# Kernel optimization log

Hardware: AMD Instinct MI355X
Metric: run time of the kernel (lower is better)

Reference implementation:

```python
import jax, jax.numpy as jnp
import numpy as np

D = 1024
NUM_ITERS = 3
EPS = 1e-6
SCALE = D ** -0.5


def rmsnorm(x, w, eps=EPS):
    return x * jax.lax.rsqrt(jnp.mean(x * x, axis=-1, keepdims=True) + eps) * w


def setup_inputs() -> dict:
    key = jax.random.key(0)
    ks = jax.random.split(key, 8)
    B, K, M, d = 8, 64, 4096, D
    w_std = d ** -0.5
    return {
        "slots": jax.random.normal(ks[0], (B, K, d), jnp.float32),
        "P": jax.random.normal(ks[1], (B, M, d), jnp.float32),
        "Wq": jax.random.normal(ks[2], (d, d), jnp.float32) * w_std,
        "Wk": jax.random.normal(ks[3], (d, d), jnp.float32) * w_std,
        "Wv": jax.random.normal(ks[4], (d, d), jnp.float32) * w_std,
        "gru_wih": jax.random.normal(ks[5], (3 * d, d), jnp.float32) * w_std,
        "gru_whh": jax.random.normal(ks[6], (3 * d, d), jnp.float32) * w_std,
        "gru_bih": jnp.zeros((3 * d,), jnp.float32),
        "gru_bhh": jnp.zeros((3 * d,), jnp.float32),
        "slot_norm_w": jnp.ones((d,), jnp.float32),
        "input_norm_w": jnp.ones((d,), jnp.float32),
    }


def gru_cell(x, h, wih, whh, bih, bhh):
    # PyTorch nn.GRUCell semantics; x, h: (..., d)
    gx = x @ wih.T + bih            # (..., 3d)
    gh = h @ whh.T + bhh
    xr, xz, xn = jnp.split(gx, 3, axis=-1)
    hr, hz, hn = jnp.split(gh, 3, axis=-1)
    r = jax.nn.sigmoid(xr + hr)
    z = jax.nn.sigmoid(xz + hz)
    n = jnp.tanh(xn + r * hn)
    return (1.0 - z) * n + z * h


def reference(slots, P, Wq, Wk, Wv, gru_wih, gru_whh, gru_bih, gru_bhh,
              slot_norm_w, input_norm_w):
    Pn = rmsnorm(P, input_norm_w)
    k_proj = Pn @ Wk.T              # (B, M, d)  (qk_layernorm=False -> identity)
    v_proj = Pn @ Wv.T              # (B, M, d)
    for _ in range(NUM_ITERS):
        sn = rmsnorm(slots, slot_norm_w)
        q_proj = sn @ Wq.T          # (B, K, d)
        scores = jnp.einsum("bkd,bmd->bkm", q_proj, k_proj) * SCALE
        attn = jax.nn.softmax(scores, axis=-2)              # compete over slots K
        attn = attn / (jnp.sum(attn, axis=-1, keepdims=True) + EPS)
        updates = jnp.einsum("bkm,bmd->bkd", attn, v_proj)
        slots = gru_cell(updates, slots, gru_wih, gru_whh, gru_bih, gru_bhh)
    return slots
```

## Files before the change

### kernel.cpp

```cpp
#include <hip/hip_runtime.h>
#include <stdint.h>

typedef _Float16 f16;
typedef __attribute__((ext_vector_type(4))) _Float16 f16x4;
typedef __attribute__((ext_vector_type(8))) _Float16 f16x8;
typedef __attribute__((ext_vector_type(4))) float f32x4;

#define EPSF 1e-6f

using as1_cvoid = const __attribute__((address_space(1))) void;
using as3_void  = __attribute__((address_space(3))) void;

__device__ __forceinline__ float blockReduceSum256(float v) {
#pragma unroll
  for (int o = 32; o > 0; o >>= 1) v += __shfl_down(v, o);
  __shared__ float red[4];
  int lane = threadIdx.x & 63, wid = threadIdx.x >> 6;
  if (lane == 0) red[wid] = v;
  __syncthreads();
  return red[0] + red[1] + red[2] + red[3];
}

__global__ __launch_bounds__(256) void cvt_f32_f16(const float* __restrict__ src,
                                                   f16* __restrict__ dst, int n) {
  int i = (blockIdx.x * 256 + threadIdx.x) * 4;
  if (i >= n) return;
  float4 v = *(const float4*)(src + i);
  f16x4 o = {(f16)v.x, (f16)v.y, (f16)v.z, (f16)v.w};
  *(f16x4*)(dst + i) = o;
}

__global__ __launch_bounds__(256) void rmsnorm_rows(const float* __restrict__ X,
                                                    const float* __restrict__ w,
                                                    f16* __restrict__ Y) {
  const size_t row = blockIdx.x;
  const int t = threadIdx.x;
  float4 v = ((const float4*)(X + row * 1024))[t];
  float tot = blockReduceSum256(v.x * v.x + v.y * v.y + v.z * v.z + v.w * v.w);
  float s = rsqrtf(tot * (1.0f / 1024.0f) + EPSF);
  float4 wv = ((const float4*)w)[t];
  f16x4 o = {(f16)(v.x * s * wv.x), (f16)(v.y * s * wv.y),
             (f16)(v.z * s * wv.z), (f16)(v.w * s * wv.w)};
  *(f16x4*)(Y + row * 1024 + t * 4) = o;
}

__global__ __launch_bounds__(256) void slots_prep(const float* __restrict__ S,
                                                  const float* __restrict__ w,
                                                  f16* __restrict__ sn,
                                                  f16* __restrict__ sraw,
                                                  float* __restrict__ rowsum) {
  const size_t row = blockIdx.x;
  const int t = threadIdx.x;
  if (t == 0) rowsum[row] = 0.f;
  float4 v = ((const float4*)(S + row * 1024))[t];
  float tot = blockReduceSum256(v.x * v.x + v.y * v.y + v.z * v.z + v.w * v.w);
  float s = rsqrtf(tot * (1.0f / 1024.0f) + EPSF);
  float4 wv = ((const float4*)w)[t];
  f16x4 a = {(f16)(v.x * s * wv.x), (f16)(v.y * s * wv.y),
             (f16)(v.z * s * wv.z), (f16)(v.w * s * wv.w)};
  f16x4 b = {(f16)v.x, (f16)v.y, (f16)v.z, (f16)v.w};
  *(f16x4*)(sn + row * 1024 + t * 4) = a;
  *(f16x4*)(sraw + row * 1024 + t * 4) = b;
}

__global__ __launch_bounds__(512) void gemm_kv(
    const f16* __restrict__ Pn, const f16* __restrict__ Wk, const f16* __restrict__ Wv,
    f16* __restrict__ kproj, f16* __restrict__ vT) {
  __shared__ f16 Al[128 * 32];
  __shared__ f16 Bkv[2][128 * 32];
  const int tid = threadIdx.x;
  const int wave = tid >> 6, lane = tid & 63;
  const int id = blockIdx.x;
  const int xcd = id & 7, slot = id >> 3;
  const int nx = slot & 7;
  const int my = xcd * 32 + (slot >> 3);
  const int m0 = my * 128, n0 = nx * 128;
  const int wsel = wave >> 2;
  const int w4 = wave & 3;
  const int wm = w4 >> 1, wn = w4 & 1;
  const int cr = lane & 15, kseg = lane >> 4;

  f32x4 acc[4][4];
  f32x4 vzero = {0.f, 0.f, 0.f, 0.f};
#pragma unroll
  for (int i = 0; i < 4; ++i)
#pragma unroll
    for (int j = 0; j < 4; ++j) acc[i][j] = vzero;

  const int off = wave * 1024 + lane * 16;
  const int sr = off >> 6, scb = off & 63;
  for (int kt = 0; kt < 32; ++kt) {
    const int k0 = kt << 5;
    {
      const char* src = (const char*)(Pn + (size_t)(m0 + sr) * 1024 + k0) + scb;
      __builtin_amdgcn_global_load_lds((as1_cvoid*)src,
                                       (as3_void*)((char*)Al + wave * 1024), 16, 0, 0);
    }
    {
      const char* src = (const char*)(Wk + (size_t)(n0 + sr) * 1024 + k0) + scb;
      __builtin_amdgcn_global_load_lds((as1_cvoid*)src,
                                       (as3_void*)((char*)&Bkv[0][0] + wave * 1024), 16, 0, 0);
    }
    {
      const char* src = (const char*)(Wv + (size_t)(n0 + sr) * 1024 + k0) + scb;
      __builtin_amdgcn_global_load_lds((as1_cvoid*)src,
                                       (as3_void*)((char*)&Bkv[1][0] + wave * 1024), 16, 0, 0);
    }
    __syncthreads();
    f16x8 af[4], bf[4];
#pragma unroll
    for (int i = 0; i < 4; ++i)
      af[i] = *(const f16x8*)&Al[(wm * 64 + i * 16 + cr) * 32 + kseg * 8];
#pragma unroll
    for (int j = 0; j < 4; ++j)
      bf[j] = *(const f16x8*)&Bkv[wsel][(wn * 64 + j * 16 + cr) * 32 + kseg * 8];
#pragma unroll
    for (int i = 0; i < 4; ++i)
#pragma unroll
      for (int j = 0; j < 4; ++j)
        acc[i][j] = __builtin_amdgcn_mfma_f32_16x16x32_f16(af[i], bf[j], acc[i][j], 0, 0, 0);
    __syncthreads();
  }

  const int cq4 = kseg * 4;
  if (wsel == 0) {
#pragma unroll
    for (int i = 0; i < 4; ++i) {
      const int rb = m0 + wm * 64 + i * 16 + cq4;
#pragma unroll
      for (int j = 0; j < 4; ++j) {
        const int gn = n0 + wn * 64 + j * 16 + cr;
#pragma unroll
        for (int r = 0; r < 4; ++r)
          kproj[(size_t)(rb + r) * 1024 + gn] = (f16)acc[i][j][r];
      }
    }
  } else {
#pragma unroll
    for (int i = 0; i < 4; ++i) {
      const int gm = m0 + wm * 64 + i * 16 + cq4;
      const int b = gm >> 12, ml = gm & 4095;
#pragma unroll
      for (int j = 0; j < 4; ++j) {
        const int gn = n0 + wn * 64 + j * 16 + cr;
        f16x4 o = {(f16)acc[i][j][0], (f16)acc[i][j][1],
                   (f16)acc[i][j][2], (f16)acc[i][j][3]};
        *(f16x4*)(vT + ((size_t)b * 1024 + gn) * 4096 + ml) = o;
      }
    }
  }
}

template <int BM, int BN, int WM, int WN, int STORE, int SPLITK>
__global__ __launch_bounds__(256) void gemm_bt(
    const f16* __restrict__ A, const f16* __restrict__ B, void* __restrict__ Cout,
    int lda, int ldb, int ldc, int K, long sA, long sB, long sC, long sY, float alpha) {
  constexpr int AM = WM / 16, AN = WN / 16;
  constexpr int NWN = BN / WN;
  constexpr int AI = BM / 64, BI = BN / 64;
  __shared__ f16 Al[BM * 32];
  __shared__ f16 Bl[BN * 32];
  const int tid = threadIdx.x;
  const int wave = tid >> 6, lane = tid & 63;
  const int wm = wave / NWN, wn = wave % NWN;
  const int z = blockIdx.z;
  const f16* Ab = A + (size_t)z * sA;
  const f16* Bb = B + (size_t)z * sB;
  const int m0 = SPLITK ? 0 : blockIdx.y * BM;
  const int n0 = blockIdx.x * BN;
  const int kbase = SPLITK ? blockIdx.y * SPLITK : 0;
  const int cr = lane & 15, kseg = lane >> 4;

  f32x4 acc[AM][AN];
  f32x4 vzero = {0.f, 0.f, 0.f, 0.f};
#pragma unroll
  for (int i = 0; i < AM; ++i)
#pragma unroll
    for (int j = 0; j < AN; ++j) acc[i][j] = vzero;

  const int nK = SPLITK ? (SPLITK >> 5) : (K >> 5);
  for (int kt = 0; kt < nK; ++kt) {
    const int k0 = kbase + (kt << 5);
#pragma unroll
    for (int it = 0; it < AI; ++it) {
      const int chunk = it * 4 + wave;
      const int off = chunk * 1024 + lane * 16;
      const int r = off >> 6, cb = off & 63;
      const char* src = (const char*)(Ab + (size_t)(m0 + r) * lda + k0) + cb;
      __builtin_amdgcn_global_load_lds((as1_cvoid*)src,
                                       (as3_void*)((char*)Al + chunk * 1024), 16, 0, 0);
    }
#pragma unroll
    for (int it = 0; it < BI; ++it) {
      const int chunk = it * 4 + wave;
      const int off = chunk * 1024 + lane * 16;
      const int r = off >> 6, cb = off & 63;
      const char* src = (const char*)(Bb + (size_t)(n0 + r) * ldb + k0) + cb;
      __builtin_amdgcn_global_load_lds((as1_cvoid*)src,
                                       (as3_void*)((char*)Bl + chunk * 1024), 16, 0, 0);
    }
    __syncthreads();
    f16x8 af[AM], bfv[AN];
#pragma unroll
    for (int i = 0; i < AM; ++i)
      af[i] = *(const f16x8*)&Al[(wm * WM + i * 16 + cr) * 32 + kseg * 8];
#pragma unroll
    for (int j = 0; j < AN; ++j)
      bfv[j] = *(const f16x8*)&Bl[(wn * WN + j * 16 + cr) * 32 + kseg * 8];
#pragma unroll
    for (int i = 0; i < AM; ++i)
#pragma unroll
      for (int j = 0; j < AN; ++j)
        acc[i][j] = __builtin_amdgcn_mfma_f32_16x16x32_f16(af[i], bfv[j], acc[i][j], 0, 0, 0);
    __syncthreads();
  }

  const int cq4 = kseg * 4;
  if constexpr (STORE == 0) {
    float* O = (float*)Cout + (size_t)z * sC + (SPLITK ? (size_t)blockIdx.y * sY : 0);
#pragma unroll
    for (int i = 0; i < AM; ++i) {
      const int rb = m0 + wm * WM + i * 16 + cq4;
#pragma unroll
      for (int j = 0; j < AN; ++j) {
        const int gn = n0 + wn * WN + j * 16 + cr;
#pragma unroll
        for (int r = 0; r < 4; ++r) O[(size_t)(rb + r) * ldc + gn] = acc[i][j][r] * alpha;
      }
    }
  } else {
    f16* O = (f16*)Cout + (size_t)z * sC;
#pragma unroll
    for (int i = 0; i < AM; ++i) {
      const int rb = m0 + wm * WM + i * 16 + cq4;
#pragma unroll
      for (int j = 0; j < AN; ++j) {
        const int gn = n0 + wn * WN + j * 16 + cr;
#pragma unroll
        for (int r = 0; r < 4; ++r)
          O[(size_t)(rb + r) * ldc + gn] = (f16)(acc[i][j][r] * alpha);
      }
    }
  }
}

__global__ __launch_bounds__(256) void attn_fused(
    const f16* __restrict__ qb, const f16* __restrict__ kproj,
    f16* __restrict__ attn, float* __restrict__ rowsum) {
  constexpr float SCALE = 0.03125f;
  __shared__ f16 Ql[64 * 32];
  __shared__ f16 Kl[128 * 32];
  __shared__ float sc[64][132];
  __shared__ f16 at[64][136];
  const int b = blockIdx.y, m0 = blockIdx.x * 128;
  const int tid = threadIdx.x;
  const int wave = tid >> 6, lane = tid & 63;
  const int cr = lane & 15, kseg = lane >> 4;

  f32x4 acc[8];
  f32x4 vzero = {0.f, 0.f, 0.f, 0.f};
#pragma unroll
  for (int j = 0; j < 8; ++j) acc[j] = vzero;

  for (int kt = 0; kt < 32; ++kt) {
    const int k0 = kt << 5;
    {
      const int off = wave * 1024 + lane * 16;
      const int r = off >> 6, cb = off & 63;
      const char* src = (const char*)(qb + (size_t)(b * 64 + r) * 1024 + k0) + cb;
      __builtin_amdgcn_global_load_lds((as1_cvoid*)src,
                                       (as3_void*)((char*)Ql + wave * 1024), 16, 0, 0);
    }
#pragma unroll
    for (int it = 0; it < 2; ++it) {
      const int chunk = it * 4 + wave;
      const int off = chunk * 1024 + lane * 16;
      const int r = off >> 6, cb = off & 63;
      const char* src = (const char*)(kproj + ((size_t)b * 4096 + m0 + r) * 1024 + k0) + cb;
      __builtin_amdgcn_global_load_lds((as1_cvoid*)src,
                                       (as3_void*)((char*)Kl + chunk * 1024), 16, 0, 0);
    }
    __syncthreads();
    f16x8 aq = *(const f16x8*)&Ql[(wave * 16 + cr) * 32 + kseg * 8];
#pragma unroll
    for (int j = 0; j < 8; ++j) {
      f16x8 bk = *(const f16x8*)&Kl[(j * 16 + cr) * 32 + kseg * 8];
      acc[j] = __builtin_amdgcn_mfma_f32_16x16x32_f16(aq, bk, acc[j], 0, 0, 0);
    }
    __syncthreads();
  }
#pragma unroll
  for (int j = 0; j < 8; ++j)
#pragma unroll
    for (int r = 0; r < 4; ++r)
      sc[wave * 16 + kseg * 4 + r][j * 16 + cr] = acc[j][r] * SCALE;
  __syncthreads();

  if (tid < 128) {
    const int m = tid;
    float v[64];
    float mx = -1e30f;
#pragma unroll
    for (int k = 0; k < 64; ++k) {
      v[k] = sc[k][m];
      mx = fmaxf(mx, v[k]);
    }
    float sum = 0.f;
#pragma unroll
    for (int k = 0; k < 64; ++k) {
      v[k] = __expf(v[k] - mx);
      sum += v[k];
    }
    float inv = 1.0f / sum;
#pragma unroll
    for (int k = 0; k < 64; ++k) at[k][m] = (f16)(v[k] * inv);
  }
  __syncthreads();

  const int k = tid >> 2, seg = tid & 3;
  float s = 0.f;
  f16x8 u[4];
#pragma unroll
  for (int c = 0; c < 4; ++c) {
    u[c] = *(const f16x8*)&at[k][seg * 32 + c * 8];
#pragma unroll
    for (int e = 0; e < 8; ++e) s += (float)u[c][e];
  }
  f16* dst = attn + ((size_t)b * 64 + k) * 4096 + m0 + seg * 32;
#pragma unroll
  for (int c = 0; c < 4; ++c) *(f16x8*)(dst + c * 8) = u[c];
  s += __shfl_down(s, 2);
  s += __shfl_down(s, 1);
  if (seg == 0) atomicAdd(&rowsum[b * 64 + k], s);
}

__global__ __launch_bounds__(256) void upd_reduce(const float* __restrict__ part,
                                                  const float* __restrict__ rowsum,
                                                  f16* __restrict__ upd) {
  const int idx = blockIdx.x * 256 + threadIdx.x;
  const int f0 = idx * 4;
  const int row = f0 >> 10;
  float4 s = *(const float4*)(part + f0);
#pragma unroll
  for (int c = 1; c < 4; ++c) {
    float4 p = *(const float4*)(part + c * 524288 + f0);
    s.x += p.x; s.y += p.y; s.z += p.z; s.w += p.w;
  }
  const float scl = 1.0f / (rowsum[row] + EPSF);
  f16x4 o = {(f16)(s.x * scl), (f16)(s.y * scl), (f16)(s.z * scl), (f16)(s.w * scl)};
  *(f16x4*)(upd + f0) = o;
}

__global__ __launch_bounds__(256) void gru_gates(const float* __restrict__ gx,
                                                 const float* __restrict__ gh,
                                                 const float* __restrict__ bih,
                                                 const float* __restrict__ bhh,
                                                 float* __restrict__ h) {
  const int idx = blockIdx.x * 256 + threadIdx.x;
  const int row = idx >> 10, col = idx & 1023;
  const float* gxr = gx + (size_t)row * 3072;
  const float* ghr = gh + (size_t)row * 3072;
  float xr = gxr[col] + bih[col];
  float xz = gxr[col + 1024] + bih[col + 1024];
  float xn = gxr[col + 2048] + bih[col + 2048];
  float hr = ghr[col] + bhh[col];
  float hz = ghr[col + 1024] + bhh[col + 1024];
  float hn = ghr[col + 2048] + bhh[col + 2048];
  float r = 1.f / (1.f + __expf(-(xr + hr)));
  float zz = 1.f / (1.f + __expf(-(xz + hz)));
  float n = tanhf(xn + r * hn);
  float hv = h[idx];
  h[idx] = (1.f - zz) * n + zz * hv;
}

extern "C" void kernel_launch(void* const* d_in, const int* in_sizes, int n_in,
                              void* d_out, int out_size, void* d_ws, size_t ws_size,
                              hipStream_t stream) {
  (void)in_sizes; (void)n_in; (void)out_size; (void)ws_size;
  const float* slots = (const float*)d_in[0];
  const float* P = (const float*)d_in[1];
  const float* Wq = (const float*)d_in[2];
  const float* Wk = (const float*)d_in[3];
  const float* Wv = (const float*)d_in[4];
  const float* wih = (const float*)d_in[5];
  const float* whh = (const float*)d_in[6];
  const float* bih = (const float*)d_in[7];
  const float* bhh = (const float*)d_in[8];
  const float* snw = (const float*)d_in[9];
  const float* inw = (const float*)d_in[10];
  float* out = (float*)d_out;
  char* ws = (char*)d_ws;

  f16* kproj = (f16*)(ws + 0);
  f16* vT    = (f16*)(ws + 67108864);
  char* rgn  = ws + 134217728;
  f16* Pn    = (f16*)rgn;
  f16* attn  = (f16*)(rgn + 0);
  float* part = (float*)(rgn + 4194304);
  f16* qb    = (f16*)(rgn + 12582912);
  f16* sn    = (f16*)(rgn + 13631488);
  f16* sbf   = (f16*)(rgn + 14680064);
  f16* upd   = (f16*)(rgn + 15728640);
  float* gxb = (float*)(rgn + 16777216);
  float* ghb = (float*)(rgn + 23068672);
  char* wr = ws + 201326592;
  f16* Wqh  = (f16*)(wr + 0);
  f16* Wkh  = (f16*)(wr + 2097152);
  f16* Wvh  = (f16*)(wr + 4194304);
  f16* wihh = (f16*)(wr + 6291456);
  f16* whhh = (f16*)(wr + 12582912);
  float* rowsum = (float*)(wr + 18874368);

  cvt_f32_f16<<<1024, 256, 0, stream>>>(Wq, Wqh, 1048576);
  cvt_f32_f16<<<1024, 256, 0, stream>>>(Wk, Wkh, 1048576);
  cvt_f32_f16<<<1024, 256, 0, stream>>>(Wv, Wvh, 1048576);
  cvt_f32_f16<<<3072, 256, 0, stream>>>(wih, wihh, 3145728);
  cvt_f32_f16<<<3072, 256, 0, stream>>>(whh, whhh, 3145728);

  rmsnorm_rows<<<32768, 256, 0, stream>>>(P, inw, Pn);

  gemm_kv<<<2048, 512, 0, stream>>>(Pn, Wkh, Wvh, kproj, vT);

  hipMemcpyAsync(out, slots, 2097152, hipMemcpyDeviceToDevice, stream);

  for (int it = 0; it < 3; ++it) {
    slots_prep<<<512, 256, 0, stream>>>(out, snw, sn, sbf, rowsum);
    gemm_bt<64, 64, 32, 32, 1, 0><<<dim3(16, 8, 1), 256, 0, stream>>>(
        sn, Wqh, qb, 1024, 1024, 1024, 1024, 0, 0, 0, 0, 1.0f);
    attn_fused<<<dim3(32, 8, 1), 256, 0, stream>>>(qb, kproj, attn, rowsum);
    gemm_bt<64, 64, 32, 32, 0, 1024><<<dim3(16, 4, 8), 256, 0, stream>>>(
        attn, vT, part, 4096, 4096, 1024, 4096, 262144, 4194304, 65536, 524288, 1.0f);
    upd_reduce<<<512, 256, 0, stream>>>(part, rowsum, upd);
    gemm_bt<64, 64, 32, 32, 0, 0><<<dim3(48, 8, 1), 256, 0, stream>>>(
        upd, wihh, gxb, 1024, 1024, 3072, 1024, 0, 0, 0, 0, 1.0f);
    gemm_bt<64, 64, 32, 32, 0, 0><<<dim3(48, 8, 1), 256, 0, stream>>>(
        sbf, whhh, ghb, 1024, 1024, 3072, 1024, 0, 0, 0, 0, 1.0f);
    gru_gates<<<2048, 256, 0, stream>>>(gxb, ghb, bih, bhh, out);
  }
}
```

Baseline: 689.2 us.

## Rewrite K/V projection GEMM with 256x256 tiles and 4-stage async LDS pipeline

```diff
diff --git a/kernel.cpp b/kernel.cpp
--- a/kernel.cpp
+++ b/kernel.cpp
@@ -63,70 +63,97 @@
   *(f16x4*)(sraw + row * 1024 + t * 4) = b;
 }
 
-__global__ __launch_bounds__(512) void gemm_kv(
+__global__ __launch_bounds__(512, 1) void gemm_kv2(
     const f16* __restrict__ Pn, const f16* __restrict__ Wk, const f16* __restrict__ Wv,
     f16* __restrict__ kproj, f16* __restrict__ vT) {
-  __shared__ f16 Al[128 * 32];
-  __shared__ f16 Bkv[2][128 * 32];
+  __shared__ f16 sm[4][2][8192];
   const int tid = threadIdx.x;
   const int wave = tid >> 6, lane = tid & 63;
+  const int cr = lane & 15, kseg = lane >> 4;
+  const int wm = wave >> 2, wn = wave & 3;
   const int id = blockIdx.x;
   const int xcd = id & 7, slot = id >> 3;
-  const int nx = slot & 7;
-  const int my = xcd * 32 + (slot >> 3);
-  const int m0 = my * 128, n0 = nx * 128;
-  const int wsel = wave >> 2;
-  const int w4 = wave & 3;
-  const int wm = w4 >> 1, wn = w4 & 1;
-  const int cr = lane & 15, kseg = lane >> 4;
-
-  f32x4 acc[4][4];
+  const int mt = xcd * 16 + (slot >> 3);
+  const int nt = slot & 7;
+  const int m0 = mt * 256, n0 = nt * 256;
+  const f16* Bmat = (n0 < 1024) ? (Wk + (size_t)n0 * 1024)
+                                : (Wv + (size_t)(n0 - 1024) * 1024);
+
+  const int line0 = tid >> 3;
+  const int L = (tid & 7) ^ (line0 & 7);
+  const int rr = (line0 << 1) + (L & 1);
+  const int slB = (L >> 1) << 4;
+  const char* aB = (const char*)(Pn + (size_t)(m0 + rr) * 1024) + slB;
+  const char* bB = (const char*)Bmat + (size_t)rr * 2048 + slB;
+  const int ldsW = wave * 1024;
+
+  const int rdOff = ((cr >> 1) << 7) + (((((kseg << 1) | (cr & 1))) ^ (cr >> 1)) << 4);
+
+  f32x4 acc[8][4];
   f32x4 vzero = {0.f, 0.f, 0.f, 0.f};
 #pragma unroll
-  for (int i = 0; i < 4; ++i)
+  for (int i = 0; i < 8; ++i)
 #pragma unroll
     for (int j = 0; j < 4; ++j) acc[i][j] = vzero;
 
-  const int off = wave * 1024 + lane * 16;
-  const int sr = off >> 6, scb = off & 63;
-  for (int kt = 0; kt < 32; ++kt) {
-    const int k0 = kt << 5;
-    {
-      const char* src = (const char*)(Pn + (size_t)(m0 + sr) * 1024 + k0) + scb;
-      __builtin_amdgcn_global_load_lds((as1_cvoid*)src,
-                                       (as3_void*)((char*)Al + wave * 1024), 16, 0, 0);
-    }
-    {
-      const char* src = (const char*)(Wk + (size_t)(n0 + sr) * 1024 + k0) + scb;
-      __builtin_amdgcn_global_load_lds((as1_cvoid*)src,
-                                       (as3_void*)((char*)&Bkv[0][0] + wave * 1024), 16, 0, 0);
-    }
-    {
-      const char* src = (const char*)(Wv + (size_t)(n0 + sr) * 1024 + k0) + scb;
-      __builtin_amdgcn_global_load_lds((as1_cvoid*)src,
-                                       (as3_void*)((char*)&Bkv[1][0] + wave * 1024), 16, 0, 0);
-    }
-    __syncthreads();
-    f16x8 af[4], bf[4];
-#pragma unroll
-    for (int i = 0; i < 4; ++i)
-      af[i] = *(const f16x8*)&Al[(wm * 64 + i * 16 + cr) * 32 + kseg * 8];
+  auto STAGE = [&](int tt) {
+    const int b = tt & 3;
+    const char* a = aB + tt * 64;
+    const char* bb = bB + tt * 64;
+    char* la = (char*)(&sm[b][0][0]) + ldsW;
+    char* lb = (char*)(&sm[b][1][0]) + ldsW;
+    __builtin_amdgcn_global_load_lds((as1_cvoid*)a, (as3_void*)la, 16, 0, 0);
+    __builtin_amdgcn_global_load_lds((as1_cvoid*)(a + 262144), (as3_void*)(la + 8192), 16, 0, 0);
+    __builtin_amdgcn_global_load_lds((as1_cvoid*)bb, (as3_void*)lb, 16, 0, 0);
+    __builtin_amdgcn_global_load_lds((as1_cvoid*)(bb + 262144), (as3_void*)(lb + 8192), 16, 0, 0);
+  };
+
+  auto COMPUTE = [&](int t) {
+    const int b = t & 3;
+    const char* A = (const char*)&sm[b][0][0];
+    const char* B = (const char*)&sm[b][1][0];
+    f16x8 bf[4];
 #pragma unroll
     for (int j = 0; j < 4; ++j)
-      bf[j] = *(const f16x8*)&Bkv[wsel][(wn * 64 + j * 16 + cr) * 32 + kseg * 8];
-#pragma unroll
-    for (int i = 0; i < 4; ++i)
+      bf[j] = *(const f16x8*)(B + (wn << 12) + (j << 10) + rdOff);
+    __builtin_amdgcn_s_setprio(1);
+#pragma unroll
+    for (int i = 0; i < 8; ++i) {
+      f16x8 af = *(const f16x8*)(A + (wm << 13) + (i << 10) + rdOff);
 #pragma unroll
       for (int j = 0; j < 4; ++j)
-        acc[i][j] = __builtin_amdgcn_mfma_f32_16x16x32_f16(af[i], bf[j], acc[i][j], 0, 0, 0);
-    __syncthreads();
-  }
-
-  const int cq4 = kseg * 4;
-  if (wsel == 0) {
-#pragma unroll
-    for (int i = 0; i < 4; ++i) {
-      const int rb = m0 + wm * 64 + i * 16 + cq4;
+        acc[i][j] = __builtin_amdgcn_mfma_f32_16x16x32_f16(af, bf[j], acc[i][j], 0, 0, 0);
+    }
+    __builtin_amdgcn_s_setprio(0);
+  };
+
+  STAGE(0); STAGE(1); STAGE(2);
+#pragma unroll 4
+  for (int t = 0; t < 29; ++t) {
+    asm volatile("s_waitcnt vmcnt(8)" ::: "memory");
+    __builtin_amdgcn_s_barrier();
+    __builtin_amdgcn_sched_barrier(0);
+    STAGE(t + 3);
+    COMPUTE(t);
+  }
+  asm volatile("s_waitcnt vmcnt(8)" ::: "memory");
+  __builtin_amdgcn_s_barrier();
+  __builtin_amdgcn_sched_barrier(0);
+  COMPUTE(29);
+  asm volatile("s_waitcnt vmcnt(4)" ::: "memory");
+  __builtin_amdgcn_s_barrier();
+  __builtin_amdgcn_sched_barrier(0);
+  COMPUTE(30);
+  asm volatile("s_waitcnt vmcnt(0)" ::: "memory");
+  __builtin_amdgcn_s_barrier();
+  __builtin_amdgcn_sched_barrier(0);
+  COMPUTE(31);
+
+  const int cq = kseg * 4;
+  if (n0 < 1024) {
+#pragma unroll
+    for (int i = 0; i < 8; ++i) {
+      const int rb = m0 + wm * 128 + i * 16 + cq;
 #pragma unroll
       for (int j = 0; j < 4; ++j) {
         const int gn = n0 + wn * 64 + j * 16 + cr;
@@ -136,13 +163,14 @@
       }
     }
   } else {
-#pragma unroll
-    for (int i = 0; i < 4; ++i) {
-      const int gm = m0 + wm * 64 + i * 16 + cq4;
+    const int nvb = n0 - 1024;
+#pragma unroll
+    for (int i = 0; i < 8; ++i) {
+      const int gm = m0 + wm * 128 + i * 16 + cq;
       const int b = gm >> 12, ml = gm & 4095;
 #pragma unroll
       for (int j = 0; j < 4; ++j) {
-        const int gn = n0 + wn * 64 + j * 16 + cr;
+        const int gn = nvb + wn * 64 + j * 16 + cr;
         f16x4 o = {(f16)acc[i][j][0], (f16)acc[i][j][1],
                    (f16)acc[i][j][2], (f16)acc[i][j][3]};
         *(f16x4*)(vT + ((size_t)b * 1024 + gn) * 4096 + ml) = o;
@@ -419,7 +447,7 @@
 
   rmsnorm_rows<<<32768, 256, 0, stream>>>(P, inw, Pn);
 
-  gemm_kv<<<2048, 512, 0, stream>>>(Pn, Wkh, Wvh, kproj, vT);
+  gemm_kv2<<<1024, 512, 0, stream>>>(Pn, Wkh, Wvh, kproj, vT);
 
   hipMemcpyAsync(out, slots, 2097152, hipMemcpyDeviceToDevice, stream);
 
```

New measurement: 673.9 us. 1.02x faster.
